# Optimization experiments

Measured on AMD Instinct MI355X. Metric: run time of the kernel, lower is better.

## Reference

```python
import jax, jax.numpy as jnp
import numpy as np

POOL_LEN = 128  # agent tokens (AdaptiveAvgPool1d output size)

def setup_inputs() -> dict:
    key = jax.random.key(0)
    ks = jax.random.split(key, 7)
    B, D, L = 8, 512, 4096
    s = 1.0 / np.sqrt(D)
    return {
        "x":  jax.random.normal(ks[0], (B, D, L), dtype=jnp.float32),
        "Wq": jax.random.normal(ks[1], (D, D), dtype=jnp.float32) * s,
        "bq": jax.random.normal(ks[2], (D,), dtype=jnp.float32) * 0.01,
        "Wk": jax.random.normal(ks[3], (D, D), dtype=jnp.float32) * s,
        "bk": jax.random.normal(ks[4], (D,), dtype=jnp.float32) * 0.01,
        "Wv": jax.random.normal(ks[5], (D, D), dtype=jnp.float32) * s,
        "bv": jax.random.normal(ks[6], (D,), dtype=jnp.float32) * 0.01,
    }

def reference(x, Wq, bq, Wk, bk, Wv, bv):
    # x: [B, D, L] channel-first, as in the torch module
    xt = jnp.swapaxes(x, -1, -2)               # [B, L, D]
    q = xt @ Wq.T + bq                         # [B, L, D]
    k = xt @ Wk.T + bk                         # [B, L, D]
    v = xt @ Wv.T + bv                         # [B, L, D]
    B, L, D = q.shape
    # AdaptiveAvgPool1d(L -> POOL_LEN): uniform segment mean since L % POOL_LEN == 0
    a = q.reshape(B, POOL_LEN, L // POOL_LEN, D).mean(axis=2)  # [B, P, D]
    # stage 1: agents attend to keys, aggregate values (no 1/sqrt(d) scaling in original)
    c = jax.nn.softmax(jnp.einsum('bpd,bld->bpl', a, k), axis=-1) @ v  # [B, P, D]
    # stage 2: queries attend to agents
    r = jax.nn.softmax(jnp.einsum('bld,bpd->blp', q, a), axis=-1) @ c  # [B, L, D]
    return jnp.swapaxes(r, -1, -2)             # [B, D, L]
```

## Files before the change

kernel.cpp:

```cpp
#include <hip/hip_runtime.h>
#include <hip/hip_fp16.h>

typedef _Float16 f16;
using frag16 = __attribute__((ext_vector_type(8))) _Float16;
using f32x4  = __attribute__((ext_vector_type(4))) float;

__device__ __forceinline__ void gload_lds16(const void* g, void* l) {
    __builtin_amdgcn_global_load_lds(
        (const __attribute__((address_space(1))) void*)g,
        (__attribute__((address_space(3))) void*)l, 16, 0, 0);
}

__global__ __launch_bounds__(256) void cvt3_f16(const float* __restrict__ Wq,
                                                const float* __restrict__ Wk,
                                                const float* __restrict__ Wv,
                                                f16* __restrict__ out) {
    int i = blockIdx.x * 256 + threadIdx.x;
    const float* src = (i < 262144) ? Wq : (i < 524288) ? Wk : Wv;
    out[i] = (f16)src[i & 262143];
}

__global__ __launch_bounds__(256) void transpose_f32_f16(const float* __restrict__ in,
                                                         f16* __restrict__ out) {
    __shared__ float t[64][65];
    const int b = blockIdx.z;
    const int d0 = blockIdx.x * 64, l0 = blockIdx.y * 64;
    const float* ip = in + (size_t)b * 512 * 4096;
    f16* op = out + (size_t)b * 4096 * 512;
#pragma unroll
    for (int it = 0; it < 4; ++it) {
        int idx = it * 256 + threadIdx.x;
        int d = idx >> 4, c4 = (idx & 15) * 4;
        const float4 v = *reinterpret_cast<const float4*>(&ip[(size_t)(d0 + d) * 4096 + l0 + c4]);
        t[d][c4] = v.x; t[d][c4 + 1] = v.y; t[d][c4 + 2] = v.z; t[d][c4 + 3] = v.w;
    }
    __syncthreads();
#pragma unroll
    for (int it = 0; it < 2; ++it) {
        int idx = it * 256 + threadIdx.x;
        int l = idx >> 3, dg = (idx & 7) * 8;
        union { f16 h[8]; uint4 u; } pk;
#pragma unroll
        for (int k = 0; k < 8; ++k) pk.h[k] = (f16)t[dg + k][l];
        *reinterpret_cast<uint4*>(&op[(size_t)(l0 + l) * 512 + d0 + dg]) = pk.u;
    }
}

__global__ __launch_bounds__(256) void softmax4096(const f16* __restrict__ S,
                                                   f16* __restrict__ P) {
    const f16* s = S + (size_t)blockIdx.x * 4096;
    f16* p = P + (size_t)blockIdx.x * 4096;
    const int tid = threadIdx.x;
    union { f16 h[16]; uint4 u[2]; } v;
    v.u[0] = *reinterpret_cast<const uint4*>(&s[tid * 16]);
    v.u[1] = *reinterpret_cast<const uint4*>(&s[tid * 16 + 8]);
    float f[16];
    float mx = -3.0e38f;
#pragma unroll
    for (int i = 0; i < 16; ++i) { f[i] = (float)v.h[i]; mx = fmaxf(mx, f[i]); }
#pragma unroll
    for (int o = 32; o; o >>= 1) mx = fmaxf(mx, __shfl_xor(mx, o));
    __shared__ float redm[4];
    __shared__ float reds[4];
    if ((tid & 63) == 0) redm[tid >> 6] = mx;
    __syncthreads();
    mx = fmaxf(fmaxf(redm[0], redm[1]), fmaxf(redm[2], redm[3]));
    float sum = 0.f;
#pragma unroll
    for (int i = 0; i < 16; ++i) { f[i] = __expf(f[i] - mx); sum += f[i]; }
#pragma unroll
    for (int o = 32; o; o >>= 1) sum += __shfl_xor(sum, o);
    if ((tid & 63) == 0) reds[tid >> 6] = sum;
    __syncthreads();
    sum = reds[0] + reds[1] + reds[2] + reds[3];
    float inv = 1.f / sum;
#pragma unroll
    for (int i = 0; i < 16; ++i) v.h[i] = (f16)(f[i] * inv);
    *reinterpret_cast<uint4*>(&p[tid * 16])     = v.u[0];
    *reinterpret_cast<uint4*>(&p[tid * 16 + 8]) = v.u[1];
}

__global__ __launch_bounds__(512) void gemm_qkv(
    const f16* __restrict__ xb, const f16* __restrict__ w,
    const float* __restrict__ bq, const float* __restrict__ bk,
    const float* __restrict__ bv,
    f16* __restrict__ qk, f16* __restrict__ vT, f16* __restrict__ a)
{
    __shared__ __align__(16) char smem[65536];
    const int tid = threadIdx.x;
    const int lane = tid & 63, wave = tid >> 6;
    const int wm = wave >> 2, wn = wave & 3;

    const int m0b = ((blockIdx.z << 3) + blockIdx.x) << 7;
    const int n0b = blockIdx.y << 7;

    const int lrow = lane & 15, kgrp = (lane >> 4) * 8;

    const int tr = tid >> 3;
    const int tcs = (((tid & 7) ^ (tr & 7)) * 8);
    const f16* gA = xb + (size_t)(m0b + tr) * 512 + tcs;
    const f16* gB = w  + (size_t)(n0b + tr) * 512 + tcs;

    f32x4 acc[4][2] = {};

    auto stage = [&](int bi, int k0) {
        char* sAp = smem + bi * 32768 + tid * 16;
        char* sBp = sAp + 16384;
        gload_lds16(gA + k0,                     sAp);
        gload_lds16(gA + (size_t)64 * 512 + k0,  sAp + 8192);
        gload_lds16(gB + k0,                     sBp);
        gload_lds16(gB + (size_t)64 * 512 + k0,  sBp + 8192);
    };
    auto compute = [&](int bi) {
        const char* base = smem + bi * 32768;
        const int swz = (lrow & 7) << 4;
        const int arow = wm * 64 + lrow;
        const int brow = wn * 32 + lrow;
#pragma unroll
        for (int kk = 0; kk < 2; ++kk) {
            const int colb = ((kgrp * 2) | (kk * 64)) ^ swz;
            frag16 af[4], bf[2];
#pragma unroll
            for (int i = 0; i < 4; ++i)
                af[i] = *(const frag16*)(base + (arow + i * 16) * 128 + colb);
#pragma unroll
            for (int j = 0; j < 2; ++j)
                bf[j] = *(const frag16*)(base + 16384 + (brow + j * 16) * 128 + colb);
#pragma unroll
            for (int i = 0; i < 4; ++i)
#pragma unroll
                for (int j = 0; j < 2; ++j)
                    acc[i][j] = __builtin_amdgcn_mfma_f32_16x16x32_f16(af[i], bf[j], acc[i][j], 0, 0, 0);
        }
    };

    stage(0, 0);
    int cur = 0;
#pragma unroll 1
    for (int t = 0; t < 7; ++t) {
        stage(cur ^ 1, (t + 1) * 64);
        asm volatile("s_waitcnt vmcnt(4)" ::: "memory");
        __builtin_amdgcn_s_barrier();
        __builtin_amdgcn_sched_barrier(0);
        compute(cur);
        __builtin_amdgcn_s_barrier();
        cur ^= 1;
    }
    asm volatile("s_waitcnt vmcnt(0)" ::: "memory");
    __builtin_amdgcn_s_barrier();
    __builtin_amdgcn_sched_barrier(0);
    compute(cur);
    __builtin_amdgcn_s_barrier();

    const int rbase = (lane >> 4) * 4;
    if (n0b < 1024) {
        const float* bptr = (n0b < 512) ? bq : bk;

        if (n0b < 512) {
            const int b = m0b >> 12;
            const int pbase = ((m0b & 4095) >> 5) + wm * 2;
#pragma unroll
            for (int j = 0; j < 2; ++j) {
                int d = n0b + wn * 32 + j * 16 + lrow;
                float badd = bptr[d];
                float s0 = 0.f, s1 = 0.f;
#pragma unroll
                for (int r = 0; r < 4; ++r) {
                    s0 += acc[0][j][r] + acc[1][j][r];
                    s1 += acc[2][j][r] + acc[3][j][r];
                }
                s0 += __shfl_xor(s0, 16); s0 += __shfl_xor(s0, 32);
                s1 += __shfl_xor(s1, 16); s1 += __shfl_xor(s1, 32);
                if (lane < 16) {
                    a[((size_t)(b * 128 + pbase)     * 512) + d] = (f16)(s0 * 0.03125f + badd);
                    a[((size_t)(b * 128 + pbase + 1) * 512) + d] = (f16)(s1 * 0.03125f + badd);
                }
            }
        }

        f16* lt = (f16*)smem;
#pragma unroll
        for (int j = 0; j < 2; ++j) {
            int col = wn * 32 + j * 16 + lrow;
            float badd = bptr[(n0b + col) & 511];
#pragma unroll
            for (int i = 0; i < 4; ++i) {
                int row = wm * 64 + i * 16 + rbase;
#pragma unroll
                for (int r = 0; r < 4; ++r)
                    lt[(row + r) * 136 + col] = (f16)(acc[i][j][r] + badd);
            }
        }
        __syncthreads();
#pragma unroll
        for (int it = 0; it < 4; ++it) {
            int cu = it * 512 + tid;
            int row = cu >> 4, c8 = (cu & 15) * 8;
            *reinterpret_cast<uint4*>(&qk[(size_t)(m0b + row) * 1024 + n0b + c8]) =
                *reinterpret_cast<const uint4*>(&lt[row * 136 + c8]);
        }
    } else {
        const int b = m0b >> 12, l0 = m0b & 4095;
        const int d0 = n0b - 1024;
        f16* vout = vT + (size_t)b * 2097152 + l0;
        float* lt = (float*)smem;
#pragma unroll
        for (int h = 0; h < 2; ++h) {
            if ((wn >> 1) == h) {
#pragma unroll
                for (int i = 0; i < 4; ++i)
#pragma unroll
                    for (int j = 0; j < 2; ++j)
#pragma unroll
                        for (int r = 0; r < 4; ++r)
                            lt[((wn & 1) * 32 + j * 16 + lrow) * 132 + wm * 64 + i * 16 + rbase + r]
                                = acc[i][j][r];
            }
            __syncthreads();
#pragma unroll
            for (int it = 0; it < 2; ++it) {
                int idx = it * 512 + tid;
                int nl = idx >> 4, mg = (idx & 15) * 8;
                int d = d0 + h * 64 + nl;
                float badd = bv[d];
                union { f16 hh[8]; uint4 u; } pk;
#pragma unroll
                for (int k = 0; k < 8; ++k)
                    pk.hh[k] = (f16)(lt[nl * 132 + mg + k] + badd);
                *reinterpret_cast<uint4*>(&vout[(size_t)d * 4096 + mg]) = pk.u;
            }
            __syncthreads();
        }
    }
}

template<bool OUT_F16>
__global__ __launch_bounds__(512) void gemm_lds(
    const f16* __restrict__ A, const f16* __restrict__ B,
    void* __restrict__ C,
    int K, int lda, int ldb, int ldc,
    long long sA, long long sB, long long sC, int splitk)
{
    __shared__ __align__(16) char smem[65536];
    const int z = blockIdx.z;
    const int batch = z / splitk;
    const int ks = z - batch * splitk;
    const int Ksub = K / splitk;
    const int kbeg = ks * Ksub;

    const f16* Ab = A + (size_t)batch * sA;
    const f16* Bb = B + (size_t)batch * sB;

    const int tid = threadIdx.x;
    const int lane = tid & 63, wave = tid >> 6;
    const int wm = wave >> 2, wn = wave & 3;
    const int m0b = blockIdx.x * 128, n0b = blockIdx.y * 128;
    const int lrow = lane & 15, kgrp = (lane >> 4) * 8;

    const int tr = tid >> 3;
    const int tcs = (((tid & 7) ^ (tr & 7)) * 8);
    const f16* gA = Ab + (size_t)(m0b + tr) * lda + tcs;
    const f16* gB = Bb + (size_t)(n0b + tr) * ldb + tcs;

    f32x4 acc[4][2] = {};

    auto stage = [&](int bi, int k0) {
        char* sAp = smem + bi * 32768 + tid * 16;
        char* sBp = sAp + 16384;
        gload_lds16(gA + k0,                     sAp);
        gload_lds16(gA + (size_t)64 * lda + k0,  sAp + 8192);
        gload_lds16(gB + k0,                     sBp);
        gload_lds16(gB + (size_t)64 * ldb + k0,  sBp + 8192);
    };
    auto compute = [&](int bi) {
        const char* base = smem + bi * 32768;
        const int swz = (lrow & 7) << 4;
        const int arow = wm * 64 + lrow;
        const int brow = wn * 32 + lrow;
#pragma unroll
        for (int kk = 0; kk < 2; ++kk) {
            const int colb = ((kgrp * 2) | (kk * 64)) ^ swz;
            frag16 af[4], bf[2];
#pragma unroll
            for (int i = 0; i < 4; ++i)
                af[i] = *(const frag16*)(base + (arow + i * 16) * 128 + colb);
#pragma unroll
            for (int j = 0; j < 2; ++j)
                bf[j] = *(const frag16*)(base + 16384 + (brow + j * 16) * 128 + colb);
#pragma unroll
            for (int i = 0; i < 4; ++i)
#pragma unroll
                for (int j = 0; j < 2; ++j)
                    acc[i][j] = __builtin_amdgcn_mfma_f32_16x16x32_f16(af[i], bf[j], acc[i][j], 0, 0, 0);
        }
    };

    stage(0, kbeg);
    int cur = 0;
    const int nt = Ksub >> 6;
#pragma unroll 1
    for (int t = 0; t < nt - 1; ++t) {
        stage(cur ^ 1, kbeg + (t + 1) * 64);
        asm volatile("s_waitcnt vmcnt(4)" ::: "memory");
        __builtin_amdgcn_s_barrier();
        __builtin_amdgcn_sched_barrier(0);
        compute(cur);
        __builtin_amdgcn_s_barrier();
        cur ^= 1;
    }
    asm volatile("s_waitcnt vmcnt(0)" ::: "memory");
    __builtin_amdgcn_s_barrier();
    __builtin_amdgcn_sched_barrier(0);
    compute(cur);
    __builtin_amdgcn_s_barrier();

    const int rbase = (lane >> 4) * 4;
    const size_t cb = (size_t)z * sC;
#pragma unroll
    for (int j = 0; j < 2; ++j) {
        int col = n0b + wn * 32 + j * 16 + lrow;
#pragma unroll
        for (int i = 0; i < 4; ++i) {
            int row = m0b + wm * 64 + i * 16 + rbase;
#pragma unroll
            for (int r = 0; r < 4; ++r) {
                float val = acc[i][j][r];
                size_t o = cb + (size_t)(row + r) * ldc + col;
                if constexpr (OUT_F16) ((f16*)C)[o] = (f16)val;
                else                   ((float*)C)[o] = val;
            }
        }
    }
}

__global__ __launch_bounds__(256) void reduce_pv(const f16* __restrict__ Pp,
                                                 f16* __restrict__ cT) {
    int idx = blockIdx.x * 256 + threadIdx.x;
    int dg = (idx & 63) * 8, p = (idx >> 6) & 127, b = idx >> 13;
    float s[8] = {};
#pragma unroll
    for (int k = 0; k < 16; ++k) {
        union { uint4 u; f16 h[8]; } v;
        v.u = *reinterpret_cast<const uint4*>(
            &Pp[(size_t)(b * 16 + k) * 65536 + p * 512 + dg]);
#pragma unroll
        for (int e = 0; e < 8; ++e) s[e] += (float)v.h[e];
    }
#pragma unroll
    for (int e = 0; e < 8; ++e)
        cT[(size_t)b * 65536 + (size_t)(dg + e) * 128 + p] = (f16)s[e];
}

__global__ __launch_bounds__(256) void attn2(
    const f16* __restrict__ qk, const f16* __restrict__ ab,
    const f16* __restrict__ cT, float* __restrict__ out)
{
    __shared__ __align__(16) char smem[69632];
    float* scr = (float*)(smem + 33280);
    f16*   P2  = (f16*)(smem + 34816);

    const int tid = threadIdx.x;
    const int lane = tid & 63, wave = tid >> 6;
    const int wm = wave >> 1, wn = wave & 1;
    const int l0 = blockIdx.x * 128;
    const int b  = blockIdx.y;
    const int lrow = lane & 15, kgrp = (lane >> 4) * 8, rbase = (lane >> 4) * 4;
    const int tr = tid >> 3, tc = (tid & 7) * 8;

    char* sAp = smem + tid * 16;
    char* sBp = smem + 16384 + tid * 16;

    const f16* gA = qk + (size_t)b * 4194304 + (size_t)(l0 + tr) * 1024 + tc;
    const f16* gB = ab + (size_t)b * 65536  + (size_t)tr * 512 + tc;

    f32x4 acc[4][4] = {};
#pragma unroll 1
    for (int k0 = 0; k0 < 512; k0 += 64) {
#pragma unroll
        for (int i = 0; i < 4; ++i) {
            gload_lds16(gA + (size_t)(i * 32) * 1024 + k0, sAp + i * 4096);
            gload_lds16(gB + (size_t)(i * 32) * 512  + k0, sBp + i * 4096);
        }
        __syncthreads();
        const f16* la = (const f16*)smem + (wm * 64 + lrow) * 64 + kgrp;
        const f16* lb = (const f16*)(smem + 16384) + (wn * 64 + lrow) * 64 + kgrp;
#pragma unroll
        for (int kk = 0; kk < 2; ++kk) {
            frag16 af[4], bf[4];
#pragma unroll
            for (int i = 0; i < 4; ++i) af[i] = *(const frag16*)(la + i * 16 * 64 + kk * 32);
#pragma unroll
            for (int j = 0; j < 4; ++j) bf[j] = *(const frag16*)(lb + j * 16 * 64 + kk * 32);
#pragma unroll
            for (int i = 0; i < 4; ++i)
#pragma unroll
                for (int j = 0; j < 4; ++j)
                    acc[i][j] = __builtin_amdgcn_mfma_f32_16x16x32_f16(af[i], bf[j], acc[i][j], 0, 0, 0);
        }
        __syncthreads();
    }

    float mx[4][4];
#pragma unroll
    for (int i = 0; i < 4; ++i)
#pragma unroll
        for (int r = 0; r < 4; ++r) {
            float m = fmaxf(fmaxf(acc[i][0][r], acc[i][1][r]),
                            fmaxf(acc[i][2][r], acc[i][3][r]));
            m = fmaxf(m, __shfl_xor(m, 1));
            m = fmaxf(m, __shfl_xor(m, 2));
            m = fmaxf(m, __shfl_xor(m, 4));
            m = fmaxf(m, __shfl_xor(m, 8));
            mx[i][r] = m;
        }
    if ((lane & 15) == 0) {
#pragma unroll
        for (int i = 0; i < 4; ++i)
#pragma unroll
            for (int r = 0; r < 4; ++r)
                scr[wn * 128 + wm * 64 + i * 16 + rbase + r] = mx[i][r];
    }
    __syncthreads();
    float rowm[4][4];
#pragma unroll
    for (int i = 0; i < 4; ++i)
#pragma unroll
        for (int r = 0; r < 4; ++r) {
            int row = wm * 64 + i * 16 + rbase + r;
            rowm[i][r] = fmaxf(scr[row], scr[128 + row]);
        }
    __syncthreads();
    float sum[4][4];
#pragma unroll
    for (int i = 0; i < 4; ++i)
#pragma unroll
        for (int r = 0; r < 4; ++r) {
            float s = 0.f;
#pragma unroll
            for (int j = 0; j < 4; ++j) {
                float p = __expf(acc[i][j][r] - rowm[i][r]);
                acc[i][j][r] = p;
                s += p;
            }
            s += __shfl_xor(s, 1);
            s += __shfl_xor(s, 2);
            s += __shfl_xor(s, 4);
            s += __shfl_xor(s, 8);
            sum[i][r] = s;
        }
    if ((lane & 15) == 0) {
#pragma unroll
        for (int i = 0; i < 4; ++i)
#pragma unroll
            for (int r = 0; r < 4; ++r)
                scr[wn * 128 + wm * 64 + i * 16 + rbase + r] = sum[i][r];
    }
    __syncthreads();
#pragma unroll
    for (int i = 0; i < 4; ++i)
#pragma unroll
        for (int r = 0; r < 4; ++r) {
            int row = wm * 64 + i * 16 + rbase + r;
            float inv = 1.f / (scr[row] + scr[128 + row]);
#pragma unroll
            for (int j = 0; j < 4; ++j)
                P2[row * 136 + wn * 64 + j * 16 + lrow] = (f16)(acc[i][j][r] * inv);
        }
    __syncthreads();

    const f16* gC = cT + (size_t)b * 65536;
    float* outb = out + (size_t)b * 512 * 4096;
#pragma unroll 1
    for (int c = 0; c < 4; ++c) {
        const int d0 = c * 128;
#pragma unroll
        for (int i = 0; i < 4; ++i) {
            gload_lds16(gC + (size_t)(d0 + tr + i * 32) * 128 + tc,      sAp + i * 4096);
            gload_lds16(gC + (size_t)(d0 + tr + i * 32) * 128 + tc + 64, sBp + i * 4096);
        }
        __syncthreads();
        f32x4 a2[4][4] = {};
#pragma unroll
        for (int half = 0; half < 2; ++half) {
            const f16* lb = (const f16*)(smem + half * 16384) + (wn * 64 + lrow) * 64 + kgrp;
            const f16* lpa = P2 + (wm * 64 + lrow) * 136 + half * 64 + kgrp;
#pragma unroll
            for (int kk = 0; kk < 2; ++kk) {
                frag16 af[4], bf[4];
#pragma unroll
                for (int i = 0; i < 4; ++i) af[i] = *(const frag16*)(lpa + i * 16 * 136 + kk * 32);
#pragma unroll
                for (int j = 0; j < 4; ++j) bf[j] = *(const frag16*)(lb + j * 16 * 64 + kk * 32);
#pragma unroll
                for (int i = 0; i < 4; ++i)
#pragma unroll
                    for (int j = 0; j < 4; ++j)
                        a2[i][j] = __builtin_amdgcn_mfma_f32_16x16x32_f16(af[i], bf[j], a2[i][j], 0, 0, 0);
            }
        }
        __syncthreads();

        float* lt = (float*)smem;
#pragma unroll
        for (int h = 0; h < 2; ++h) {
            if (wn == h) {
#pragma unroll
                for (int i = 0; i < 4; ++i)
#pragma unroll
                    for (int j = 0; j < 4; ++j)
#pragma unroll
                        for (int r = 0; r < 4; ++r)
                            lt[(j * 16 + lrow) * 132 + wm * 64 + i * 16 + rbase + r] = a2[i][j][r];
            }
            __syncthreads();
#pragma unroll
            for (int it = 0; it < 8; ++it) {
                int idx = it * 256 + tid;
                int nl = idx >> 5, mq = (idx & 31) * 4;
                float4 v = *reinterpret_cast<const float4*>(&lt[nl * 132 + mq]);
                *reinterpret_cast<float4*>(&outb[(size_t)(d0 + h * 64 + nl) * 4096 + l0 + mq]) = v;
            }
            __syncthreads();
        }
    }
}

extern "C" void kernel_launch(void* const* d_in, const int* in_sizes, int n_in,
                              void* d_out, int out_size, void* d_ws, size_t ws_size,
                              hipStream_t stream) {
    const float* x  = (const float*)d_in[0];
    const float* Wq = (const float*)d_in[1];
    const float* bq = (const float*)d_in[2];
    const float* Wk = (const float*)d_in[3];
    const float* bk = (const float*)d_in[4];
    const float* Wv = (const float*)d_in[5];
    const float* bv = (const float*)d_in[6];
    float* out = (float*)d_out;

    const size_t o_xb = 0;
    const size_t o_qk = 33554432;
    const size_t o_vT = 100663296;
    const size_t o_w  = 134217728;
    const size_t o_ab = o_w + 1572864;
    const size_t o_cT = o_ab + 1048576;
    const size_t o_S  = o_cT + 1048576;
    const size_t o_P  = o_S + 16777216;
    const size_t need = o_P + 8388608;
    if (ws_size < need) return;

    char* ws = (char*)d_ws;
    f16* xb   = (f16*)(ws + o_xb);
    f16* qk   = (f16*)(ws + o_qk);
    f16* vT   = (f16*)(ws + o_vT);
    f16* wqkv = (f16*)(ws + o_w);
    f16* ab   = (f16*)(ws + o_ab);
    f16* cT   = (f16*)(ws + o_cT);
    f16* Sb   = (f16*)(ws + o_S);
    f16* Pp   = (f16*)(ws + o_S);
    f16* Pb   = (f16*)(ws + o_P);

    cvt3_f16<<<3072, 256, 0, stream>>>(Wq, Wk, Wv, wqkv);

    transpose_f32_f16<<<dim3(8, 64, 8), 256, 0, stream>>>(x, xb);

    gemm_qkv<<<dim3(8, 12, 32), 512, 0, stream>>>(xb, wqkv, bq, bk, bv, qk, vT, ab);

    gemm_lds<true><<<dim3(1, 32, 8), 512, 0, stream>>>(
        ab, qk + 512, Sb, 512, 512, 1024, 4096, 65536LL, 4194304LL, 524288LL, 1);

    softmax4096<<<1024, 256, 0, stream>>>(Sb, Pb);

    gemm_lds<true><<<dim3(1, 4, 128), 512, 0, stream>>>(
        Pb, vT, Pp, 4096, 4096, 4096, 512, 524288LL, 2097152LL, 65536LL, 16);
    reduce_pv<<<256, 256, 0, stream>>>(Pp, cT);

    attn2<<<dim3(32, 8), 256, 0, stream>>>(qk, ab, cT, out);
}
```

Measured before the change: 160.3 us.

## Fuse x transpose and fp16 conversion into QKV GEMM A-tile loading

Removes the separate transpose_f32_f16 kernel and the xb workspace. The QKV GEMM now reads channel-first fp32 x directly into registers, converts it to fp16 and writes swizzled A tiles into LDS. The pipeline becomes register-staged for A with a full vmcnt(0) wait each iteration. This avoids a 64MB read plus 32MB write round trip through HBM. In exchange, each of the 12 column blocks re-reads fp32 x with strided loads, and the main loop has less overlap.

Result: slower. 164.0 us (+2.3%).

```diff
diff --git a/kernel.cpp b/kernel.cpp
--- a/kernel.cpp
+++ b/kernel.cpp
@@ -18,32 +18,6 @@
     int i = blockIdx.x * 256 + threadIdx.x;
     const float* src = (i < 262144) ? Wq : (i < 524288) ? Wk : Wv;
     out[i] = (f16)src[i & 262143];
-}
-
-__global__ __launch_bounds__(256) void transpose_f32_f16(const float* __restrict__ in,
-                                                         f16* __restrict__ out) {
-    __shared__ float t[64][65];
-    const int b = blockIdx.z;
-    const int d0 = blockIdx.x * 64, l0 = blockIdx.y * 64;
-    const float* ip = in + (size_t)b * 512 * 4096;
-    f16* op = out + (size_t)b * 4096 * 512;
-#pragma unroll
-    for (int it = 0; it < 4; ++it) {
-        int idx = it * 256 + threadIdx.x;
-        int d = idx >> 4, c4 = (idx & 15) * 4;
-        const float4 v = *reinterpret_cast<const float4*>(&ip[(size_t)(d0 + d) * 4096 + l0 + c4]);
-        t[d][c4] = v.x; t[d][c4 + 1] = v.y; t[d][c4 + 2] = v.z; t[d][c4 + 3] = v.w;
-    }
-    __syncthreads();
-#pragma unroll
-    for (int it = 0; it < 2; ++it) {
-        int idx = it * 256 + threadIdx.x;
-        int l = idx >> 3, dg = (idx & 7) * 8;
-        union { f16 h[8]; uint4 u; } pk;
-#pragma unroll
-        for (int k = 0; k < 8; ++k) pk.h[k] = (f16)t[dg + k][l];
-        *reinterpret_cast<uint4*>(&op[(size_t)(l0 + l) * 512 + d0 + dg]) = pk.u;
-    }
 }
 
 __global__ __launch_bounds__(256) void softmax4096(const f16* __restrict__ S,
@@ -81,7 +55,7 @@
 }
 
 __global__ __launch_bounds__(512) void gemm_qkv(
-    const f16* __restrict__ xb, const f16* __restrict__ w,
+    const float* __restrict__ x, const f16* __restrict__ w,
     const float* __restrict__ bq, const float* __restrict__ bk,
     const float* __restrict__ bv,
     f16* __restrict__ qk, f16* __restrict__ vT, f16* __restrict__ a)
@@ -96,20 +70,37 @@
 
     const int lrow = lane & 15, kgrp = (lane >> 4) * 8;
 
+    const int b   = m0b >> 12;
+    const int l0m = m0b & 4095;
+
+    const float* gx = x + (size_t)b * 2097152 + l0m + 2 * lane;
+    const int row0 = 2 * lane, row1 = row0 + 1;
+
     const int tr = tid >> 3;
     const int tcs = (((tid & 7) ^ (tr & 7)) * 8);
-    const f16* gA = xb + (size_t)(m0b + tr) * 512 + tcs;
-    const f16* gB = w  + (size_t)(n0b + tr) * 512 + tcs;
+    const f16* gB = w + (size_t)(n0b + tr) * 512 + tcs;
 
     f32x4 acc[4][2] = {};
-
-    auto stage = [&](int bi, int k0) {
-        char* sAp = smem + bi * 32768 + tid * 16;
-        char* sBp = sAp + 16384;
-        gload_lds16(gA + k0,                     sAp);
-        gload_lds16(gA + (size_t)64 * 512 + k0,  sAp + 8192);
-        gload_lds16(gB + k0,                     sBp);
-        gload_lds16(gB + (size_t)64 * 512 + k0,  sBp + 8192);
+    float2 areg[8];
+
+    auto loadA = [&](int k0) {
+#pragma unroll
+        for (int e = 0; e < 8; ++e)
+            areg[e] = *reinterpret_cast<const float2*>(
+                gx + (size_t)(k0 + wave * 8 + e) * 4096);
+    };
+    auto writeA = [&](int bi) {
+        char* base = smem + bi * 32768;
+        union { f16 h[8]; uint4 u; } p0, p1;
+#pragma unroll
+        for (int e = 0; e < 8; ++e) { p0.h[e] = (f16)areg[e].x; p1.h[e] = (f16)areg[e].y; }
+        *reinterpret_cast<uint4*>(base + row0 * 128 + ((wave ^ (row0 & 7)) * 16)) = p0.u;
+        *reinterpret_cast<uint4*>(base + row1 * 128 + ((wave ^ (row1 & 7)) * 16)) = p1.u;
+    };
+    auto stageB = [&](int bi, int k0) {
+        char* sBp = smem + bi * 32768 + 16384 + tid * 16;
+        gload_lds16(gB + k0,                    sBp);
+        gload_lds16(gB + (size_t)64 * 512 + k0, sBp + 8192);
     };
     auto compute = [&](int bi) {
         const char* base = smem + bi * 32768;
@@ -134,31 +125,30 @@
         }
     };
 
-    stage(0, 0);
+    loadA(0);
+    stageB(0, 0);
     int cur = 0;
 #pragma unroll 1
-    for (int t = 0; t < 7; ++t) {
-        stage(cur ^ 1, (t + 1) * 64);
-        asm volatile("s_waitcnt vmcnt(4)" ::: "memory");
+    for (int t = 0; t < 8; ++t) {
+        asm volatile("s_waitcnt vmcnt(0)" ::: "memory");
+        writeA(cur);
+        __syncthreads();
+        if (t < 7) {
+            loadA((t + 1) * 64);
+            stageB(cur ^ 1, (t + 1) * 64);
+        }
+        compute(cur);
         __builtin_amdgcn_s_barrier();
         __builtin_amdgcn_sched_barrier(0);
-        compute(cur);
-        __builtin_amdgcn_s_barrier();
         cur ^= 1;
     }
-    asm volatile("s_waitcnt vmcnt(0)" ::: "memory");
-    __builtin_amdgcn_s_barrier();
-    __builtin_amdgcn_sched_barrier(0);
-    compute(cur);
-    __builtin_amdgcn_s_barrier();
 
     const int rbase = (lane >> 4) * 4;
     if (n0b < 1024) {
         const float* bptr = (n0b < 512) ? bq : bk;
 
         if (n0b < 512) {
-            const int b = m0b >> 12;
-            const int pbase = ((m0b & 4095) >> 5) + wm * 2;
+            const int pbase = (l0m >> 5) + wm * 2;
 #pragma unroll
             for (int j = 0; j < 2; ++j) {
                 int d = n0b + wn * 32 + j * 16 + lrow;
@@ -200,9 +190,8 @@
                 *reinterpret_cast<const uint4*>(&lt[row * 136 + c8]);
         }
     } else {
-        const int b = m0b >> 12, l0 = m0b & 4095;
         const int d0 = n0b - 1024;
-        f16* vout = vT + (size_t)b * 2097152 + l0;
+        f16* vout = vT + (size_t)b * 2097152 + l0m;
         float* lt = (float*)smem;
 #pragma unroll
         for (int h = 0; h < 2; ++h) {
@@ -537,7 +526,6 @@
     const float* bv = (const float*)d_in[6];
     float* out = (float*)d_out;
 
-    const size_t o_xb = 0;
     const size_t o_qk = 33554432;
     const size_t o_vT = 100663296;
     const size_t o_w  = 134217728;
@@ -549,7 +537,6 @@
     if (ws_size < need) return;
 
     char* ws = (char*)d_ws;
-    f16* xb   = (f16*)(ws + o_xb);
     f16* qk   = (f16*)(ws + o_qk);
     f16* vT   = (f16*)(ws + o_vT);
     f16* wqkv = (f16*)(ws + o_w);
@@ -561,9 +548,7 @@
 
     cvt3_f16<<<3072, 256, 0, stream>>>(Wq, Wk, Wv, wqkv);
 
-    transpose_f32_f16<<<dim3(8, 64, 8), 256, 0, stream>>>(x, xb);
-
-    gemm_qkv<<<dim3(8, 12, 32), 512, 0, stream>>>(xb, wqkv, bq, bk, bv, qk, vT, ab);
+    gemm_qkv<<<dim3(8, 12, 32), 512, 0, stream>>>(x, wqkv, bq, bk, bv, qk, vT, ab);
 
     gemm_lds<true><<<dim3(1, 32, 8), 512, 0, stream>>>(
         ab, qk + 512, Sb, 512, 512, 1024, 4096, 65536LL, 4194304LL, 524288LL, 1);
```
